# Optimization experiments

Measured on AMD Instinct MI355X. Metric: run time of the kernel, lower is better.

The kernel has to match this reference:

```python
import jax, jax.numpy as jnp
import numpy as np


def setup_inputs() -> dict:
    key = jax.random.key(0)
    ks = jax.random.split(key, 5)
    B, N, Fin, Fout = 8, 2048, 512, 512
    stdv = 1.0 / np.sqrt(Fout)
    w_stdv = 1.0 / np.sqrt(Fin)
    x = jax.random.normal(ks[0], (B, N, Fin), dtype=jnp.float32)
    weight = jax.random.uniform(ks[1], (Fin, Fout), dtype=jnp.float32, minval=-stdv, maxval=stdv)
    bias = jax.random.uniform(ks[2], (Fout,), dtype=jnp.float32, minval=-stdv, maxval=stdv)
    w_one = jax.random.uniform(ks[3], (Fin, Fin), dtype=jnp.float32, minval=-w_stdv, maxval=w_stdv)
    w_two = jax.random.uniform(ks[4], (Fin, Fin), dtype=jnp.float32, minval=-w_stdv, maxval=w_stdv)
    return {"x": x, "weight": weight, "bias": bias, "w_one": w_one, "w_two": w_two}


def reference(x, weight, bias, w_one, w_two):
    # x: [B, N, Fin]
    support = jnp.einsum('bnf,fo->bno', x, weight)          # [B, N, Fout]
    phi_one = jnp.einsum('ef,bnf->ben', w_one, x)           # [B, Fin, N]
    phi_two = jnp.einsum('ef,bnf->ben', w_two, x)           # [B, Fin, N]
    adj = jnp.einsum('ben,bem->bnm', phi_one, phi_two)      # [B, N, N]
    adj = jax.nn.softmax(adj, axis=1)                        # softmax over dim=1 (columns)
    out = jnp.einsum('bnm,bmo->bno', adj, support)           # [B, N, Fout]
    return out + bias
```

## Files before the change

### kernel.cpp

```cpp
#include <hip/hip_runtime.h>
#include <math.h>

#define BB 8
#define NN 2048
#define FF 512
#define LOG2E 1.4426950408889634f

typedef __attribute__((ext_vector_type(8))) short short8;
typedef __attribute__((ext_vector_type(4))) float floatx4;
typedef __attribute__((ext_vector_type(2))) float float2v;
typedef __attribute__((ext_vector_type(2))) __bf16 bf16x2;

__device__ __forceinline__ unsigned short f2bf(float f) {
    union { float f; unsigned u; } v; v.f = f;
    unsigned r = v.u + 0x7FFFu + ((v.u >> 16) & 1u);
    return (unsigned short)(r >> 16);
}

__device__ __forceinline__ float fexp2(float x) {
#if __has_builtin(__builtin_amdgcn_exp2f)
    return __builtin_amdgcn_exp2f(x);
#else
    return __expf(x * 0.69314718056f);
#endif
}

__device__ __forceinline__ void pk_store(unsigned short* p0, unsigned short* p1,
                                         float a, float b) {
    union { bf16x2 h; unsigned short s[2]; } u;
    float2v v; v.x = a; v.y = b;
    u.h = __builtin_convertvector(v, bf16x2);
    *p0 = u.s[0]; *p1 = u.s[1];
}

#define BAR() __builtin_amdgcn_s_barrier()
#define LGKM0() do { asm volatile("s_waitcnt lgkmcnt(0)" ::: "memory"); \
                     __builtin_amdgcn_sched_barrier(0); } while (0)
#define GLDS(src, dst) __builtin_amdgcn_global_load_lds( \
    (const __attribute__((address_space(1))) void*)(src), \
    (__attribute__((address_space(3))) void*)(dst), 16, 0, 0)
#define VMW(n) asm volatile("s_waitcnt vmcnt(" #n ")" ::: "memory")

template<int M_REP, int MODE>
__global__ __launch_bounds__(512) void gemm256(
    const unsigned short* __restrict__ A, const unsigned short* __restrict__ B,
    void* __restrict__ Cv, const float* __restrict__ bias, float* __restrict__ Dsum,
    int K, int a_ld, int b_ld, int ldc,
    long a_batch, long b_batch, long c_batch)
{
    constexpr int BM    = M_REP * 32;
    constexpr int LA    = BM / 128;
    constexpr int ASLOT = BM * 32;
    constexpr int BSLOT = 256 * 32;
    __shared__ __align__(16) unsigned short SH[4 * ASLOT + 4 * BSLOT];

    const int tid  = threadIdx.x;
    const int wave = tid >> 6;
    const int lane = tid & 63;
    const int wr   = wave >> 2;
    const int wc   = wave & 3;
    const int fl   = lane & 15;
    const int quad = lane >> 4;

    const int gx = gridDim.x, gy = gridDim.y;
    int flat = blockIdx.x + gx * (blockIdx.y + gy * blockIdx.z);
    const int cpx = (gx * gy * gridDim.z) >> 3;
    if (cpx > 0) flat = (flat & 7) * cpx + (flat >> 3);
    const int bx = flat % gx;
    const int rest = flat / gx;
    const int by = rest % gy;
    const int bz = rest / gy;

    const int m0 = by * BM;
    const int n0 = bx * 256;

    const unsigned short* Aptr = A + (long)bz * a_batch + (long)m0 * a_ld;
    const unsigned short* Bptr = B + (long)bz * b_batch + (long)n0 * b_ld;

    int offA[LA], offB[2];
    #pragma unroll
    for (int i = 0; i < LA; ++i) {
        const int cl = i * 512 + tid;
        const int r = cl >> 2, s = cl & 3;
        offA[i] = r * a_ld + (s ^ ((r >> 1) & 3)) * 8;
    }
    #pragma unroll
    for (int i = 0; i < 2; ++i) {
        const int cl = i * 512 + tid;
        const int r = cl >> 2, s = cl & 3;
        offB[i] = r * b_ld + (s ^ ((r >> 1) & 3)) * 8;
    }

    const int swz = (quad ^ ((fl >> 1) & 3)) * 8;
    const int aRd = (wr * (M_REP * 16) + fl) * 32 + swz;
    const int bRd = (wc * 64 + fl) * 32 + swz;

    auto sA = [&](int kh, int db, int kb) {
        #pragma unroll
        for (int i = 0; i < LA; ++i)
            GLDS(Aptr + kb + offA[i], &SH[(kh * 2 + db) * ASLOT + (i * 512 + tid) * 8]);
    };
    auto sB = [&](int kh, int db, int kb) {
        #pragma unroll
        for (int i = 0; i < 2; ++i)
            GLDS(Bptr + kb + offB[i], &SH[4 * ASLOT + (kh * 2 + db) * BSLOT + (i * 512 + tid) * 8]);
    };

    floatx4 acc[M_REP][4] = {};
    short8 af[M_REP], bf[4];

    auto RA = [&](int kh, int db) {
        const unsigned short* b = &SH[(kh * 2 + db) * ASLOT + aRd];
        #pragma unroll
        for (int m = 0; m < M_REP; ++m) af[m] = *(const short8*)(b + m * 512);
    };
    auto RB4 = [&](int kh, int db) {
        const unsigned short* b = &SH[4 * ASLOT + (kh * 2 + db) * BSLOT + bRd];
        bf[0] = *(const short8*)(b);
        bf[1] = *(const short8*)(b + 512);
        bf[2] = *(const short8*)(b + 1024);
        bf[3] = *(const short8*)(b + 1536);
    };
    auto MCF = [&]() {
        __builtin_amdgcn_s_setprio(1);
        #pragma unroll
        for (int m = 0; m < M_REP; ++m)
            #pragma unroll
            for (int j = 0; j < 4; ++j)
                acc[m][j] = __builtin_amdgcn_mfma_f32_16x16x32_bf16(af[m], bf[j], acc[m][j], 0, 0, 0);
        __builtin_amdgcn_s_setprio(0);
    };

    const int nt = K >> 6;
    const int ni = nt >> 1;

    sA(0, 0, 0);  sB(0, 0, 0);
    sA(1, 0, 32); sB(1, 0, 32);
    sA(0, 1, 64); sB(0, 1, 64);
    if constexpr (LA == 2) VMW(8); else VMW(6);
    BAR();

    for (int i = 0; i < ni; ++i) {
        const bool last = (i == ni - 1);
        const int kb1 = (2 * i + 1) * 64, kb2 = kb1 + 64, kb3 = kb2 + 64;

        RA(0, 0); RB4(0, 0);
        sA(1, 1, kb1 + 32); sB(1, 1, kb1 + 32);
        if constexpr (LA == 2) VMW(8); else VMW(6);
        BAR(); LGKM0(); MCF(); BAR();

        RA(1, 0); RB4(1, 0);
        if (!last) {
            sA(0, 0, kb2); sB(0, 0, kb2);
            if constexpr (LA == 2) VMW(8); else VMW(6);
        } else {
            if constexpr (LA == 2) VMW(4); else VMW(3);
        }
        BAR(); LGKM0(); MCF(); BAR();

        RA(0, 1); RB4(0, 1);
        if (!last) {
            sA(1, 0, kb2 + 32); sB(1, 0, kb2 + 32);
            if constexpr (LA == 2) VMW(8); else VMW(6);
        } else {
            VMW(0);
        }
        BAR(); LGKM0(); MCF(); BAR();

        RA(1, 1); RB4(1, 1);
        if (!last) {
            sA(0, 1, kb3); sB(0, 1, kb3);
            if constexpr (LA == 2) VMW(8); else VMW(6);
        }
        BAR(); LGKM0(); MCF(); BAR();
    }

    const int wmg = m0 + wr * (M_REP * 16);
    const int wcol = wc * 64;

    if constexpr (MODE == 0) {
        float* Cb = (float*)Cv + (long)bz * c_batch;
        #pragma unroll
        for (int n = 0; n < 4; ++n) {
            const int ng = n0 + wcol + n * 16 + fl;
            const float badd = bias ? bias[ng] : 0.0f;
            #pragma unroll
            for (int m = 0; m < M_REP; ++m) {
                const int mg = wmg + m * 16 + quad * 4;
                #pragma unroll
                for (int r = 0; r < 4; ++r)
                    Cb[(long)(mg + r) * ldc + ng] = acc[m][n][r] + badd;
            }
        }
    } else {
        unsigned short* Cb = (unsigned short*)Cv + (long)bz * c_batch;
        if constexpr (MODE == 2) {
            float* Db = Dsum + (long)bz * NN;
            #pragma unroll
            for (int m = 0; m < M_REP; ++m)
                #pragma unroll
                for (int n = 0; n < 4; ++n)
                    #pragma unroll
                    for (int r = 0; r < 4; ++r)
                        acc[m][n][r] = fexp2(acc[m][n][r]);
            #pragma unroll
            for (int n = 0; n < 4; ++n) {
                float csum = 0.f;
                #pragma unroll
                for (int m = 0; m < M_REP; ++m)
                    csum += acc[m][n][0] + acc[m][n][1] + acc[m][n][2] + acc[m][n][3];
                csum += __shfl_xor(csum, 16);
                csum += __shfl_xor(csum, 32);
                if (quad == 0) atomicAdd(&Db[n0 + wcol + n * 16 + fl], csum);
            }
        }
        __syncthreads();
        #pragma unroll
        for (int m = 0; m < M_REP; ++m) {
            const int rowb = wr * (M_REP * 16) + m * 16 + quad * 4;
            #pragma unroll
            for (int n = 0; n < 4; ++n) {
                const int pc = (wcol + n * 16 + fl) ^ (quad << 4);
                #pragma unroll
                for (int r = 0; r < 4; ++r)
                    SH[(rowb + r) * 256 + pc] = f2bf(acc[m][n][r]);
            }
        }
        __syncthreads();
        #pragma unroll
        for (int k = 0; k < M_REP * 2; ++k) {
            const int idx = k * 512 + tid;
            const int row = idx >> 5, c8 = (idx & 31) * 8;
            const int lcol = c8 ^ (((row >> 2) & 3) << 4);
            short8 vv = *(const short8*)&SH[row * 256 + lcol];
            *(short8*)&Cb[(long)(m0 + row) * ldc + n0 + c8] = vv;
        }
    }
}

__global__ __launch_bounds__(256) void gemm128_bt(
    const unsigned short* __restrict__ A, const unsigned short* __restrict__ B,
    unsigned short* __restrict__ C, int K, int a_ld, int b_ld, int ldc)
{
    __shared__ __align__(16) unsigned short Alds[128 * 64];
    __shared__ __align__(16) unsigned short Blds[128 * 64];

    const int tid  = threadIdx.x;
    const int wave = tid >> 6;
    const int lane = tid & 63;
    const int m0 = blockIdx.y * 128;
    const int n0 = blockIdx.x * 128;

    const unsigned short* Aptr = A + (long)m0 * a_ld;
    const unsigned short* Bptr = B + (long)n0 * b_ld;

    const int wm   = (wave >> 1) * 64;
    const int wn   = (wave & 1) * 64;
    const int fl   = lane & 15;
    const int quad = lane >> 4;

    int offA[4], offB[4], cb[4];
    #pragma unroll
    for (int issue = 0; issue < 4; ++issue) {
        const int cbase = issue * 256 + wave * 64;
        const int c = cbase + lane;
        const int row = c >> 3;
        const int kq = ((c & 7) ^ ((c >> 3) & 7)) * 8;
        offA[issue] = row * a_ld + kq;
        offB[issue] = row * b_ld + kq;
        cb[issue] = cbase * 8;
    }

    floatx4 acc[4][4] = {};

    for (int k0 = 0; k0 < K; k0 += 64) {
        #pragma unroll
        for (int issue = 0; issue < 4; ++issue) {
            GLDS(Aptr + offA[issue], &Alds[cb[issue] + lane * 8]);
            GLDS(Bptr + offB[issue], &Blds[cb[issue] + lane * 8]);
        }
        Aptr += 64; Bptr += 64;
        __syncthreads();

        #pragma unroll
        for (int s = 0; s < 2; ++s) {
            short8 af[4], bfr[4];
            const int slot = ((s * 4 + quad) ^ (fl & 7)) * 8;
            #pragma unroll
            for (int i = 0; i < 4; ++i)
                af[i] = *(const short8*)&Alds[(wm + i * 16 + fl) * 64 + slot];
            #pragma unroll
            for (int j = 0; j < 4; ++j)
                bfr[j] = *(const short8*)&Blds[(wn + j * 16 + fl) * 64 + slot];
            #pragma unroll
            for (int i = 0; i < 4; ++i)
                #pragma unroll
                for (int j = 0; j < 4; ++j)
                    acc[i][j] = __builtin_amdgcn_mfma_f32_16x16x32_bf16(af[i], bfr[j], acc[i][j], 0, 0, 0);
        }
        __syncthreads();
    }

    #pragma unroll
    for (int j = 0; j < 4; ++j) {
        const int ng = n0 + wn + j * 16 + fl;
        #pragma unroll
        for (int i = 0; i < 4; ++i) {
            const int mg = m0 + wm + i * 16 + quad * 4;
            pk_store(&C[(long)(mg + 0) * ldc + ng], &C[(long)(mg + 1) * ldc + ng],
                     acc[i][j][0], acc[i][j][1]);
            pk_store(&C[(long)(mg + 2) * ldc + ng], &C[(long)(mg + 3) * ldc + ng],
                     acc[i][j][2], acc[i][j][3]);
        }
    }
}

__global__ __launch_bounds__(256) void prep_all(
    const float* __restrict__ x, const float* __restrict__ w1,
    const float* __restrict__ w2, const float* __restrict__ w,
    unsigned short* __restrict__ xb, unsigned short* __restrict__ w1T,
    unsigned short* __restrict__ w2T, unsigned short* __restrict__ wT,
    float* __restrict__ Dsum)
{
    __shared__ float tl[32][33];
    int b = blockIdx.x;
    if (b < 4096) {
        const long i = ((long)b * 256 + threadIdx.x) * 8;
        float4 a = *(const float4*)(x + i);
        float4 c = *(const float4*)(x + i + 4);
        union { bf16x2 h[4]; short8 s8; } u;
        float2v v;
        v.x = a.x; v.y = a.y; u.h[0] = __builtin_convertvector(v, bf16x2);
        v.x = a.z; v.y = a.w; u.h[1] = __builtin_convertvector(v, bf16x2);
        v.x = c.x; v.y = c.y; u.h[2] = __builtin_convertvector(v, bf16x2);
        v.x = c.z; v.y = c.w; u.h[3] = __builtin_convertvector(v, bf16x2);
        *(short8*)(xb + i) = u.s8;
        return;
    }
    b -= 4096;
    if (b < 768) {
        const float* in; unsigned short* out; float sc = 1.0f;
        const int seg = b >> 8, t = b & 255;
        if (seg == 0)      { in = w1; out = w1T; sc = LOG2E; }
        else if (seg == 1) { in = w2; out = w2T; }
        else               { in = w;  out = wT; }
        const int tx = threadIdx.x & 31, ty = threadIdx.x >> 5;
        const int x0 = (t & 15) * 32, y0 = (t >> 4) * 32;
        #pragma unroll
        for (int k = 0; k < 32; k += 8)
            tl[ty + k][tx] = in[(long)(y0 + ty + k) * FF + x0 + tx];
        __syncthreads();
        #pragma unroll
        for (int k = 0; k < 32; k += 8)
            out[(long)(x0 + ty + k) * FF + y0 + tx] = f2bf(tl[tx][ty + k] * sc);
        return;
    }
    b -= 768;
    Dsum[(long)b * 256 + threadIdx.x] = 0.0f;
}

__global__ __launch_bounds__(256) void scale_transpose(
    const unsigned short* __restrict__ Call, const float* __restrict__ D,
    unsigned short* __restrict__ supT, int batch0)
{
    __shared__ float t[32][33];
    __shared__ float rD[32];
    const int tx = threadIdx.x & 31, ty = threadIdx.x >> 5;
    const int mt = blockIdx.x * 32, ot = blockIdx.y * 32;
    const int b = batch0 + blockIdx.z;
    const unsigned short* Cb = Call + (long)b * NN * 1024;
    unsigned short* Tb = supT + (long)b * NN * FF;
    if (threadIdx.x < 32) rD[threadIdx.x] = 1.0f / D[(long)b * NN + mt + threadIdx.x];
    __syncthreads();
    #pragma unroll
    for (int k = 0; k < 32; k += 8) {
        unsigned short u = Cb[(long)(mt + ty + k) * 1024 + 512 + ot + tx];
        union { unsigned uu; float f; } cv; cv.uu = ((unsigned)u) << 16;
        t[ty + k][tx] = cv.f;
    }
    __syncthreads();
    #pragma unroll
    for (int k = 0; k < 32; k += 8)
        Tb[(long)(ot + ty + k) * NN + mt + tx] = f2bf(t[tx][ty + k] * rD[tx]);
}

extern "C" void kernel_launch(void* const* d_in, const int* in_sizes, int n_in,
                              void* d_out, int out_size, void* d_ws, size_t ws_size,
                              hipStream_t stream)
{
    const float* x      = (const float*)d_in[0];
    const float* weight = (const float*)d_in[1];
    const float* bias   = (const float*)d_in[2];
    const float* w_one  = (const float*)d_in[3];
    const float* w_two  = (const float*)d_in[4];
    float* out = (float*)d_out;

    const long NF  = (long)NN * FF;
    const long NN2 = (long)NN * NN;
    const long CROW = 1024;

    char* p = (char*)d_ws;
    unsigned short* xb    = (unsigned short*)p; p += (size_t)BB * NF * 2;
    unsigned short* Wg1   = (unsigned short*)p; p += (size_t)1024 * FF * 2;
    unsigned short* w1T   = (unsigned short*)p; p += (size_t)FF * FF * 2;
    unsigned short* w2T   = (unsigned short*)p; p += (size_t)FF * FF * 2;
    unsigned short* Call  = (unsigned short*)p; p += (size_t)BB * NN * CROW * 2;
    unsigned short* supT  = (unsigned short*)p; p += (size_t)BB * NF * 2;
    float*          Dsum  = (float*)p;          p += (size_t)BB * NN * 4;
    unsigned short* E     = (unsigned short*)p;
    unsigned short* Vw  = Wg1;
    unsigned short* wTb = Wg1 + (size_t)FF * FF;

    const size_t fixed = (size_t)(p - (char*)d_ws);
    const bool full = ws_size >= fixed + (size_t)BB * NN2 * 2;

    dim3 blk(256), blk5(512);

    prep_all<<<dim3(4928), blk, 0, stream>>>(
        x, w_one, w_two, weight, xb, w1T, w2T, wTb, Dsum);

    gemm128_bt<<<dim3(FF / 128, FF / 128), blk, 0, stream>>>(
        w2T, w1T, Vw, FF, FF, FF, FF);

    gemm256<8, 1><<<dim3(1024 / 256, NN / 256, BB), blk5, 0, stream>>>(
        xb, Wg1, Call, nullptr, nullptr, FF,
        FF, FF, (int)CROW, NF, 0, NN * CROW);

    if (full) {
        gemm256<8, 2><<<dim3(NN / 256, NN / 256, BB), blk5, 0, stream>>>(
            Call, xb, E, nullptr, Dsum, FF,
            (int)CROW, FF, NN, NN * CROW, NF, NN2);
        scale_transpose<<<dim3(NN / 32, FF / 32, BB), blk, 0, stream>>>(Call, Dsum, supT, 0);
        gemm256<4, 0><<<dim3(FF / 256, NN / 128, BB), blk5, 0, stream>>>(
            E, supT, out, bias, nullptr, NN,
            NN, NN, FF, NN2, NF, NF);
    } else {
        for (int b = 0; b < BB; ++b) {
            const unsigned short* Cb = Call + (size_t)b * NN * CROW;
            gemm256<8, 2><<<dim3(NN / 256, NN / 256, 1), blk5, 0, stream>>>(
                Cb, xb + (size_t)b * NF, E, nullptr, Dsum + (size_t)b * NN, FF,
                (int)CROW, FF, NN, 0, 0, 0);
            scale_transpose<<<dim3(NN / 32, FF / 32, 1), blk, 0, stream>>>(Call, Dsum, supT, b);
            gemm256<4, 0><<<dim3(FF / 256, NN / 128, 1), blk5, 0, stream>>>(
                E, supT + (size_t)b * NF, out + (size_t)b * NF, bias, nullptr, NN,
                NN, NN, FF, 0, 0, 0);
        }
    }
}
```

Before: 215.4 us.

## Halve gemm256 LDS footprint with a two-stage pipeline and staged epilogue

Shrinks the GEMM kernel's shared memory from four A/B stage slots to two by switching from a four-slot, 64-wide K loop to a simple double-buffered loop over 32-wide K steps. Each iteration prefetches the tile two steps ahead and runs fewer barriers per tile. The bf16 epilogue now goes through LDS in 128-row halves so the buffer only needs to hold 128x256 elements. The aim is to cut LDS use so more blocks fit per CU; the cost is a shallower prefetch depth, which may expose global-load latency.

```diff
diff --git a/kernel.cpp b/kernel.cpp
--- a/kernel.cpp
+++ b/kernel.cpp
@@ -52,7 +52,10 @@
     constexpr int LA    = BM / 128;
     constexpr int ASLOT = BM * 32;
     constexpr int BSLOT = 256 * 32;
-    __shared__ __align__(16) unsigned short SH[4 * ASLOT + 4 * BSLOT];
+    constexpr int SLOTS = 2 * ASLOT + 2 * BSLOT;
+    constexpr int REST  = (MODE == 0) ? 0 : 128 * 256;
+    constexpr int LSZ   = SLOTS > REST ? SLOTS : REST;
+    __shared__ __align__(16) unsigned short SH[LSZ];
 
     const int tid  = threadIdx.x;
     const int wave = tid >> 6;
@@ -95,27 +98,27 @@
     const int aRd = (wr * (M_REP * 16) + fl) * 32 + swz;
     const int bRd = (wc * 64 + fl) * 32 + swz;
 
-    auto sA = [&](int kh, int db, int kb) {
+    auto sA = [&](int p, int kb) {
         #pragma unroll
         for (int i = 0; i < LA; ++i)
-            GLDS(Aptr + kb + offA[i], &SH[(kh * 2 + db) * ASLOT + (i * 512 + tid) * 8]);
+            GLDS(Aptr + kb + offA[i], &SH[p * ASLOT + (i * 512 + tid) * 8]);
     };
-    auto sB = [&](int kh, int db, int kb) {
+    auto sB = [&](int p, int kb) {
         #pragma unroll
         for (int i = 0; i < 2; ++i)
-            GLDS(Bptr + kb + offB[i], &SH[4 * ASLOT + (kh * 2 + db) * BSLOT + (i * 512 + tid) * 8]);
+            GLDS(Bptr + kb + offB[i], &SH[2 * ASLOT + p * BSLOT + (i * 512 + tid) * 8]);
     };
 
     floatx4 acc[M_REP][4] = {};
     short8 af[M_REP], bf[4];
 
-    auto RA = [&](int kh, int db) {
-        const unsigned short* b = &SH[(kh * 2 + db) * ASLOT + aRd];
+    auto RA = [&](int p) {
+        const unsigned short* b = &SH[p * ASLOT + aRd];
         #pragma unroll
         for (int m = 0; m < M_REP; ++m) af[m] = *(const short8*)(b + m * 512);
     };
-    auto RB4 = [&](int kh, int db) {
-        const unsigned short* b = &SH[4 * ASLOT + (kh * 2 + db) * BSLOT + bRd];
+    auto RB4 = [&](int p) {
+        const unsigned short* b = &SH[2 * ASLOT + p * BSLOT + bRd];
         bf[0] = *(const short8*)(b);
         bf[1] = *(const short8*)(b + 512);
         bf[2] = *(const short8*)(b + 1024);
@@ -131,48 +134,30 @@
         __builtin_amdgcn_s_setprio(0);
     };
 
-    const int nt = K >> 6;
-    const int ni = nt >> 1;
-
-    sA(0, 0, 0);  sB(0, 0, 0);
-    sA(1, 0, 32); sB(1, 0, 32);
-    sA(0, 1, 64); sB(0, 1, 64);
-    if constexpr (LA == 2) VMW(8); else VMW(6);
+    const int nt = K >> 5;
+
+    sA(0, 0);  sB(0, 0);
+    sA(1, 32); sB(1, 32);
+    if constexpr (LA == 2) VMW(4); else VMW(3);
     BAR();
 
-    for (int i = 0; i < ni; ++i) {
-        const bool last = (i == ni - 1);
-        const int kb1 = (2 * i + 1) * 64, kb2 = kb1 + 64, kb3 = kb2 + 64;
-
-        RA(0, 0); RB4(0, 0);
-        sA(1, 1, kb1 + 32); sB(1, 1, kb1 + 32);
-        if constexpr (LA == 2) VMW(8); else VMW(6);
-        BAR(); LGKM0(); MCF(); BAR();
-
-        RA(1, 0); RB4(1, 0);
-        if (!last) {
-            sA(0, 0, kb2); sB(0, 0, kb2);
-            if constexpr (LA == 2) VMW(8); else VMW(6);
-        } else {
+    for (int t = 0; t < nt; ++t) {
+        const int p = t & 1;
+        RA(p); RB4(p);
+        LGKM0();
+        BAR();
+        const bool more = (t + 2 < nt);
+        if (more) {
+            sA(p, (t + 2) * 32);
+            sB(p, (t + 2) * 32);
+        }
+        MCF();
+        if (more) {
             if constexpr (LA == 2) VMW(4); else VMW(3);
-        }
-        BAR(); LGKM0(); MCF(); BAR();
-
-        RA(0, 1); RB4(0, 1);
-        if (!last) {
-            sA(1, 0, kb2 + 32); sB(1, 0, kb2 + 32);
-            if constexpr (LA == 2) VMW(8); else VMW(6);
-        } else {
+        } else if (t + 1 < nt) {
             VMW(0);
         }
-        BAR(); LGKM0(); MCF(); BAR();
-
-        RA(1, 1); RB4(1, 1);
-        if (!last) {
-            sA(0, 1, kb3); sB(0, 1, kb3);
-            if constexpr (LA == 2) VMW(8); else VMW(6);
-        }
-        BAR(); LGKM0(); MCF(); BAR();
+        BAR();
     }
 
     const int wmg = m0 + wr * (M_REP * 16);
@@ -214,26 +199,32 @@
                 if (quad == 0) atomicAdd(&Db[n0 + wcol + n * 16 + fl], csum);
             }
         }
-        __syncthreads();
-        #pragma unroll
-        for (int m = 0; m < M_REP; ++m) {
-            const int rowb = wr * (M_REP * 16) + m * 16 + quad * 4;
-            #pragma unroll
-            for (int n = 0; n < 4; ++n) {
-                const int pc = (wcol + n * 16 + fl) ^ (quad << 4);
+        constexpr int HALVES = BM / 128;
+        #pragma unroll
+        for (int h = 0; h < HALVES; ++h) {
+            __syncthreads();
+            if (HALVES == 1 || wr == h) {
                 #pragma unroll
-                for (int r = 0; r < 4; ++r)
-                    SH[(rowb + r) * 256 + pc] = f2bf(acc[m][n][r]);
+                for (int m = 0; m < M_REP; ++m) {
+                    const int lrow = (HALVES == 2 ? 0 : wr * 64) + m * 16 + quad * 4;
+                    #pragma unroll
+                    for (int n = 0; n < 4; ++n) {
+                        const int pc = (wcol + n * 16 + fl) ^ (quad << 4);
+                        #pragma unroll
+                        for (int r = 0; r < 4; ++r)
+                            SH[(lrow + r) * 256 + pc] = f2bf(acc[m][n][r]);
+                    }
+                }
             }
-        }
-        __syncthreads();
-        #pragma unroll
-        for (int k = 0; k < M_REP * 2; ++k) {
-            const int idx = k * 512 + tid;
-            const int row = idx >> 5, c8 = (idx & 31) * 8;
-            const int lcol = c8 ^ (((row >> 2) & 3) << 4);
-            short8 vv = *(const short8*)&SH[row * 256 + lcol];
-            *(short8*)&Cb[(long)(m0 + row) * ldc + n0 + c8] = vv;
+            __syncthreads();
+            #pragma unroll
+            for (int k = 0; k < 8; ++k) {
+                const int idx = k * 512 + tid;
+                const int row = idx >> 5, c8 = (idx & 31) * 8;
+                const int lcol = c8 ^ (((row >> 2) & 3) << 4);
+                short8 vv = *(const short8*)&SH[row * 256 + lcol];
+                *(short8*)&Cb[(long)(m0 + h * 128 + row) * ldc + n0 + c8] = vv;
+            }
         }
     }
 }
```

After: 223.3 us. 3.7% more time.
